# Kernel tuning notes

Measured on AMD Instinct MI355X. Metric: run time of the kernel, lower is better.

## Reference

```python
import jax, jax.numpy as jnp
import numpy as np


def setup_inputs() -> dict:
    key = jax.random.key(0)
    k1, k2, k3 = jax.random.split(key, 3)
    B, C, H, W = 8, 256, 64, 64
    K = jax.random.normal(k1, (B, C, H, W), dtype=jnp.float32)
    Q = jax.random.normal(k2, (B, C, H, W), dtype=jnp.float32)
    V = jax.random.normal(k3, (B, C, H, W), dtype=jnp.float32)
    return {"K": K, "Q": Q, "V": V}


def reference(K, Q, V):
    # K, Q: [b, dim, h, w]; V: [b, v_dim, h, w]
    b, dim, h, w = K.shape
    v_dim = V.shape[1]
    hw = h * w
    Qf = jnp.transpose(K.reshape(b, dim, hw), (0, 2, 1)) * 0  # placeholder removed below
    Qf = jnp.transpose(Q.reshape(b, dim, hw), (0, 2, 1))  # [b, hw, dim]
    Kf = K.reshape(b, dim, hw)                              # [b, dim, hw]
    Vf = jnp.transpose(V.reshape(b, v_dim, hw), (0, 2, 1))  # [b, hw, v_dim]
    scores = jnp.einsum('bqd,bdk->bqk', Qf, Kf)             # [b, hw_q, hw_k]
    # NOTE: softmax over the QUERY axis (dim=1), matching the torch code
    att = jax.nn.softmax(scores, axis=1)
    out = jnp.einsum('bqk,bkv->bqv', att, Vf)               # [b, hw, v_dim]
    out = out.reshape(b, h, w, v_dim)
    return jnp.transpose(out, (0, 3, 1, 2))                 # [b, v_dim, h, w]
```

## Files before the change

### kernel.cpp

```cpp
#include <hip/hip_runtime.h>

#define HW   4096
#define DIM  256
#define NB   8

typedef short bf16x8 __attribute__((ext_vector_type(8)));
typedef short s16x4  __attribute__((ext_vector_type(4)));
typedef float f32x4  __attribute__((ext_vector_type(4)));
typedef float f32x16 __attribute__((ext_vector_type(16)));
typedef unsigned int u32;
typedef unsigned int u32_g __attribute__((address_space(1)));
typedef unsigned int u32_l __attribute__((address_space(3)));

__device__ __forceinline__ void split_bf16(float x, short& hi, short& lo) {
    unsigned u  = __builtin_bit_cast(unsigned, x);
    unsigned rh = (u + 0x7FFFu + ((u >> 16) & 1u)) >> 16;
    hi = (short)rh;
    float hf  = __builtin_bit_cast(float, rh << 16);
    float rem = x - hf;
    unsigned u2 = __builtin_bit_cast(unsigned, rem);
    unsigned rl = (u2 + 0x7FFFu + ((u2 >> 16) & 1u)) >> 16;
    lo = (short)rl;
}

__device__ __forceinline__ f32x4 mfma16(bf16x8 a, bf16x8 b, f32x4 c) {
    return __builtin_amdgcn_mfma_f32_16x16x32_bf16(a, b, c, 0, 0, 0);
}
__device__ __forceinline__ f32x16 mfma32(bf16x8 a, bf16x8 b, f32x16 c) {
    return __builtin_amdgcn_mfma_f32_32x32x16_bf16(a, b, c, 0, 0, 0);
}

__device__ __forceinline__ void gload16(const void* g, void* l) {
    __builtin_amdgcn_global_load_lds((const u32_g*)g, (u32_l*)l, 16, 0, 0);
}


extern "C" __global__ void __launch_bounds__(256)
pass0_T(const float* __restrict__ src, short* __restrict__ dsth,
        short* __restrict__ dstl)
{
    __shared__ __attribute__((aligned(16))) short TH[16][264];
    __shared__ __attribute__((aligned(16))) short TL[16][264];
    const int b   = blockIdx.y;
    const int hw0 = blockIdx.x * 16;
    const int t   = threadIdx.x;
    const float* sb = src + (size_t)b * DIM * HW;

    {
        const int rl = t & 15;
        const int dl = t >> 4;
        #pragma unroll
        for (int dp = 0; dp < 16; ++dp) {
            int d = dl + dp * 16;
            float x = sb[(size_t)d * HW + hw0 + rl];
            short h, l; split_bf16(x, h, l);
            TH[rl][d] = h; TL[rl][d] = l;
        }
    }
    __syncthreads();

    const int r   = t >> 4;
    const int c0  = (t & 15) * 2;
    const int swz = (r & 7) << 4;
    size_t rowbyte = ((size_t)b * HW + hw0 + r) * (size_t)(DIM * 2);
    char* dh = (char*)dsth + rowbyte;
    char* dl = (char*)dstl + rowbyte;
    #pragma unroll
    for (int j = 0; j < 2; ++j) {
        int cb  = (c0 + j) * 16;
        int cbs = cb ^ swz;
        *(f32x4*)(dh + cbs) = *(const f32x4*)((const char*)&TH[r][0] + cb);
        *(f32x4*)(dl + cbs) = *(const f32x4*)((const char*)&TL[r][0] + cb);
    }
}

extern "C" __global__ void __launch_bounds__(256)
pass0_V(const float* __restrict__ V, short* __restrict__ v2)
{
    const int b = blockIdx.y, v = blockIdx.x, t = threadIdx.x;
    const float* sv = V + ((size_t)b * DIM + v) * HW + t * 16;
    #pragma unroll
    for (int s = 0; s < 2; ++s) {
        f32x4 x0 = *(const f32x4*)(sv + s * 8);
        f32x4 x1 = *(const f32x4*)(sv + s * 8 + 4);
        s16x4 h0, l0, h1, l1;
        #pragma unroll
        for (int j = 0; j < 4; ++j) {
            short h, l;
            split_bf16(x0[j], h, l); h0[j] = h; l0[j] = l;
            split_bf16(x1[j], h, l); h1[j] = h; l1[j] = l;
        }
        short* dp = v2 + (((size_t)b * 512 + (size_t)(t * 2 + s)) * DIM + v) * 16;
        *(s16x4*)(dp + 0)  = h0;
        *(s16x4*)(dp + 4)  = h1;
        *(s16x4*)(dp + 8)  = l0;
        *(s16x4*)(dp + 12) = l1;
    }
}

extern "C" __global__ void __launch_bounds__(256, 2)
k2_stats(const short* __restrict__ KTh, const short* __restrict__ KTl,
         const short* __restrict__ QTh, const short* __restrict__ QTl,
         float* __restrict__ m_out, float* __restrict__ il_out)
{
    __shared__ __attribute__((aligned(16))) short QH[2][32][256];
    __shared__ __attribute__((aligned(16))) short QL[2][32][256];

    const int b    = blockIdx.y;
    const int k0b  = blockIdx.x * 64;
    const int t    = threadIdx.x;
    const int lane = t & 63;
    const int w    = t >> 6;
    const int g    = lane >> 4;
    const int lq   = lane & 15;

    bf16x8 kh[8], kl[8];
    {
        const int krow = k0b + w * 16 + lq;
        const char* rh = (const char*)KTh + ((size_t)b * HW + krow) * 512;
        const char* rl = (const char*)KTl + ((size_t)b * HW + krow) * 512;
        const int swz = (lq & 7) << 4;
        #pragma unroll
        for (int ds = 0; ds < 8; ++ds) {
            int cb = (64 * ds + 16 * g) ^ swz;
            kh[ds] = *(const bf16x8*)(rh + cb);
            kl[ds] = *(const bf16x8*)(rl + cb);
        }
    }

    const char* qhbase = (const char*)QTh + (size_t)b * HW * 512;
    const char* qlbase = (const char*)QTl + (size_t)b * HW * 512;
    auto stage = [&](int bi, int q0) {
        #pragma unroll
        for (int j = 0; j < 4; ++j) {
            int c   = (j << 2) + w;
            int off = c * 1024 + lane * 16;
            gload16(qhbase + (size_t)q0 * 512 + off, (char*)&QH[bi][0][0] + c * 1024);
            gload16(qlbase + (size_t)q0 * 512 + off, (char*)&QL[bi][0][0] + c * 1024);
        }
    };

    float mr[4], lr[4];
    #pragma unroll
    for (int r = 0; r < 4; ++r) { mr[r] = -3.0e38f; lr[r] = 0.0f; }

    stage(0, 0);
    __syncthreads();

    for (int it = 0; it < 128; ++it) {
        const int cur = it & 1;
        if (it + 1 < 128) stage(cur ^ 1, (it + 1) * 32);

        #pragma unroll
        for (int qt = 0; qt < 2; ++qt) {
            const int qr = qt * 16 + lq;
            const char* bhr = (const char*)&QH[cur][qr][0];
            const char* blr = (const char*)&QL[cur][qr][0];
            const int swzq = (qr & 7) << 4;
            f32x4 acc = {0.f, 0.f, 0.f, 0.f};
            #pragma unroll
            for (int ds = 0; ds < 8; ++ds) {
                int cb = (64 * ds + 16 * g) ^ swzq;
                bf16x8 bh = *(const bf16x8*)(bhr + cb);
                bf16x8 bl = *(const bf16x8*)(blr + cb);
                acc = mfma16(kh[ds], bh, acc);
                acc = mfma16(kh[ds], bl, acc);
                acc = mfma16(kl[ds], bh, acc);
            }
            #pragma unroll
            for (int r = 0; r < 4; ++r) {
                float s = acc[r];
                if (s > mr[r]) {
                    lr[r] = lr[r] * __expf(mr[r] - s) + 1.0f;
                    mr[r] = s;
                } else {
                    lr[r] += __expf(s - mr[r]);
                }
            }
        }
        __syncthreads();
    }

    #pragma unroll
    for (int r = 0; r < 4; ++r) {
        float m = mr[r], l = lr[r];
        #pragma unroll
        for (int off = 1; off < 16; off <<= 1) {
            float m2 = __shfl_xor(m, off);
            float l2 = __shfl_xor(l, off);
            float mn = fmaxf(m, m2);
            l = l * __expf(m - mn) + l2 * __expf(m2 - mn);
            m = mn;
        }
        if (lq == 0) {
            int kg = k0b + w * 16 + g * 4 + r;
            m_out[b * HW + kg]  = m;
            il_out[b * HW + kg] = 1.0f / l;
        }
    }
}

extern "C" __global__ void __launch_bounds__(256, 2)
k2_out(const short* __restrict__ KTh, const short* __restrict__ KTl,
       const short* __restrict__ QTh, const short* __restrict__ QTl,
       const short* __restrict__ V2,
       const float* __restrict__ m_in, const float* __restrict__ il_in,
       float* __restrict__ out)
{
    __shared__ __attribute__((aligned(16))) short KH[2][32][256];
    __shared__ __attribute__((aligned(16))) short KL[2][32][256];
    __shared__ __attribute__((aligned(16))) short PH[64][32];
    __shared__ __attribute__((aligned(16))) short PL[64][32];

    const int b    = blockIdx.y;
    const int q0   = blockIdx.x * 64;
    const int t    = threadIdx.x;
    const int lane = t & 63;
    const int w    = t >> 6;
    const int g    = lane >> 4;
    const int lq   = lane & 15;
    const int g2   = lane >> 5;
    const int l32  = lane & 31;

    bf16x8 qh[8], ql[8];
    {
        const int qrow = q0 + w * 16 + lq;
        const char* rh = (const char*)QTh + ((size_t)b * HW + qrow) * 512;
        const char* rl = (const char*)QTl + ((size_t)b * HW + qrow) * 512;
        const int swz = (lq & 7) << 4;
        #pragma unroll
        for (int ds = 0; ds < 8; ++ds) {
            int cb = (64 * ds + 16 * g) ^ swz;
            qh[ds] = *(const bf16x8*)(rh + cb);
            ql[ds] = *(const bf16x8*)(rl + cb);
        }
    }

    const char* khbase = (const char*)KTh + (size_t)b * HW * 512;
    const char* klbase = (const char*)KTl + (size_t)b * HW * 512;
    auto stage = [&](int bi, int k0) {
        #pragma unroll
        for (int j = 0; j < 4; ++j) {
            int c   = (j << 2) + w;
            int off = c * 1024 + lane * 16;
            gload16(khbase + (size_t)k0 * 512 + off, (char*)&KH[bi][0][0] + c * 1024);
            gload16(klbase + (size_t)k0 * 512 + off, (char*)&KL[bi][0][0] + c * 1024);
        }
    };

    f32x16 acc[2][2];
    #pragma unroll
    for (int i = 0; i < 2; ++i)
        #pragma unroll
        for (int j = 0; j < 2; ++j)
            #pragma unroll
            for (int e = 0; e < 16; ++e) acc[i][j][e] = 0.0f;

    const float* mB  = m_in  + b * HW;
    const float* ilB = il_in + b * HW;

    stage(0, 0);
    __syncthreads();

    for (int it = 0; it < 128; ++it) {
        const int cur = it & 1;
        const int k0  = it * 32;
        if (it + 1 < 128) stage(cur ^ 1, k0 + 32);

        f32x4 sacc[2];
        #pragma unroll
        for (int kt = 0; kt < 2; ++kt) { f32x4 z = {0.f,0.f,0.f,0.f}; sacc[kt] = z; }
        const int swzk = (lq & 7) << 4;
        const char* ahr0 = (const char*)&KH[cur][lq][0];
        const char* ahr1 = (const char*)&KH[cur][16 + lq][0];
        const char* alr0 = (const char*)&KL[cur][lq][0];
        const char* alr1 = (const char*)&KL[cur][16 + lq][0];
        #pragma unroll
        for (int ds = 0; ds < 8; ++ds) {
            int cb = (64 * ds + 16 * g) ^ swzk;
            {
                bf16x8 ah = *(const bf16x8*)(ahr0 + cb);
                bf16x8 al = *(const bf16x8*)(alr0 + cb);
                sacc[0] = mfma16(ah, qh[ds], sacc[0]);
                sacc[0] = mfma16(ah, ql[ds], sacc[0]);
                sacc[0] = mfma16(al, qh[ds], sacc[0]);
            }
            {
                bf16x8 ah = *(const bf16x8*)(ahr1 + cb);
                bf16x8 al = *(const bf16x8*)(alr1 + cb);
                sacc[1] = mfma16(ah, qh[ds], sacc[1]);
                sacc[1] = mfma16(ah, ql[ds], sacc[1]);
                sacc[1] = mfma16(al, qh[ds], sacc[1]);
            }
        }

        {
            const int qc   = w * 16 + lq;
            const int pswz = ((qc >> 1) & 3) << 4;
            #pragma unroll
            for (int kt = 0; kt < 2; ++kt) {
                int kg = k0 + kt * 16 + g * 4;
                f32x4 m4  = *(const f32x4*)&mB[kg];
                f32x4 il4 = *(const f32x4*)&ilB[kg];
                s16x4 ph, pl;
                #pragma unroll
                for (int r = 0; r < 4; ++r) {
                    float p = __expf(sacc[kt][r] - m4[r]) * il4[r];
                    short h, l; split_bf16(p, h, l);
                    ph[r] = h; pl[r] = l;
                }
                int cb = (32 * kt + 8 * g) ^ pswz;
                *(s16x4*)((char*)&PH[0][0] + qc * 64 + cb) = ph;
                *(s16x4*)((char*)&PL[0][0] + qc * 64 + cb) = pl;
            }
        }
        __syncthreads();

        #pragma unroll
        for (int kc = 0; kc < 2; ++kc) {
            bf16x8 pbh[2], pbl[2];
            #pragma unroll
            for (int qt = 0; qt < 2; ++qt) {
                int prow = qt * 32 + l32;
                int cb = (32 * kc + 16 * g2) ^ (((prow >> 1) & 3) << 4);
                pbh[qt] = *(const bf16x8*)((const char*)&PH[0][0] + prow * 64 + cb);
                pbl[qt] = *(const bf16x8*)((const char*)&PL[0][0] + prow * 64 + cb);
            }
            const int seg = (k0 >> 3) + kc * 2 + g2;
            #pragma unroll
            for (int mt = 0; mt < 2; ++mt) {
                int v = w * 64 + mt * 32 + l32;
                const short* vp = V2 + (((size_t)b * 512 + seg) * DIM + v) * 16;
                bf16x8 vh = *(const bf16x8*)(vp);
                bf16x8 vl = *(const bf16x8*)(vp + 8);
                #pragma unroll
                for (int qt = 0; qt < 2; ++qt) {
                    acc[mt][qt] = mfma32(vh, pbh[qt], acc[mt][qt]);
                    acc[mt][qt] = mfma32(vh, pbl[qt], acc[mt][qt]);
                    acc[mt][qt] = mfma32(vl, pbh[qt], acc[mt][qt]);
                }
            }
        }
        __syncthreads();
    }

    float* ob = out + (size_t)b * DIM * HW;
    #pragma unroll
    for (int mt = 0; mt < 2; ++mt)
        #pragma unroll
        for (int qt = 0; qt < 2; ++qt)
            #pragma unroll
            for (int r = 0; r < 16; ++r) {
                int v = w * 64 + mt * 32 + (r & 3) + 8 * (r >> 2) + 4 * g2;
                int q = q0 + qt * 32 + l32;
                ob[(size_t)v * HW + q] = acc[mt][qt][r];
            }
}

extern "C" __global__ void __launch_bounds__(256, 1)
k_stats(const float* __restrict__ K, const float* __restrict__ Q,
        float* __restrict__ m_out, float* __restrict__ il_out)
{
    __shared__ __attribute__((aligned(16))) short KtH[64][264];
    __shared__ __attribute__((aligned(16))) short KtL[64][264];
    __shared__ __attribute__((aligned(16))) short QtH[32][264];
    __shared__ __attribute__((aligned(16))) short QtL[32][264];

    const int b = blockIdx.y, k0 = blockIdx.x * 64, t = threadIdx.x;
    const int lane = t & 63, w = t >> 6, g = lane >> 4, lq = lane & 15;
    const float* Kb = K + (size_t)b * DIM * HW;
    const float* Qb = Q + (size_t)b * DIM * HW;

    {
        const int kk = t & 63, d0 = t >> 6;
        #pragma unroll 4
        for (int pass = 0; pass < 64; ++pass) {
            int d = d0 + pass * 4;
            float x = Kb[(size_t)d * HW + k0 + kk];
            short h, l; split_bf16(x, h, l);
            KtH[kk][d] = h; KtL[kk][d] = l;
        }
    }
    float mr[4], lr[4];
    #pragma unroll
    for (int r = 0; r < 4; ++r) { mr[r] = -3.0e38f; lr[r] = 0.0f; }

    for (int q0 = 0; q0 < HW; q0 += 32) {
        __syncthreads();
        {
            const int qq = t & 31, d0 = t >> 5;
            #pragma unroll 4
            for (int pass = 0; pass < 32; ++pass) {
                int d = d0 + pass * 8;
                float x = Qb[(size_t)d * HW + q0 + qq];
                short h, l; split_bf16(x, h, l);
                QtH[qq][d] = h; QtL[qq][d] = l;
            }
        }
        __syncthreads();
        #pragma unroll
        for (int qt = 0; qt < 2; ++qt) {
            f32x4 acc = {0.f, 0.f, 0.f, 0.f};
            #pragma unroll
            for (int ds = 0; ds < 8; ++ds) {
                const int dof = ds * 32 + g * 8;
                bf16x8 ah = *(const bf16x8*)&KtH[w * 16 + lq][dof];
                bf16x8 al = *(const bf16x8*)&KtL[w * 16 + lq][dof];
                bf16x8 bh = *(const bf16x8*)&QtH[qt * 16 + lq][dof];
                bf16x8 bl = *(const bf16x8*)&QtL[qt * 16 + lq][dof];
                acc = mfma16(ah, bh, acc);
                acc = mfma16(ah, bl, acc);
                acc = mfma16(al, bh, acc);
            }
            #pragma unroll
            for (int r = 0; r < 4; ++r) {
                float s = acc[r];
                if (s > mr[r]) { lr[r] = lr[r] * __expf(mr[r] - s) + 1.0f; mr[r] = s; }
                else lr[r] += __expf(s - mr[r]);
            }
        }
    }
    #pragma unroll
    for (int r = 0; r < 4; ++r) {
        float m = mr[r], l = lr[r];
        #pragma unroll
        for (int off = 1; off < 16; off <<= 1) {
            float m2 = __shfl_xor(m, off), l2 = __shfl_xor(l, off);
            float mn = fmaxf(m, m2);
            l = l * __expf(m - mn) + l2 * __expf(m2 - mn);
            m = mn;
        }
        if (lq == 0) {
            int kg = k0 + w * 16 + g * 4 + r;
            m_out[b * HW + kg] = m;
            il_out[b * HW + kg] = 1.0f / l;
        }
    }
}

extern "C" __global__ void __launch_bounds__(256, 1)
k_attn_out(const float* __restrict__ K, const float* __restrict__ Q,
           const float* __restrict__ V,
           const float* __restrict__ m_in, const float* __restrict__ il_in,
           float* __restrict__ out)
{
    __shared__ __attribute__((aligned(16))) short QtH[64][264];
    __shared__ __attribute__((aligned(16))) short QtL[64][264];
    __shared__ __attribute__((aligned(16))) short KtH[32][264];
    __shared__ __attribute__((aligned(16))) short KtL[32][264];
    __shared__ __attribute__((aligned(16))) short PtH[64][40];
    __shared__ __attribute__((aligned(16))) short PtL[64][40];

    const int b = blockIdx.y, q0 = blockIdx.x * 64, t = threadIdx.x;
    const int lane = t & 63, w = t >> 6, g = lane >> 4, lq = lane & 15;
    const int g2 = lane >> 5, l32 = lane & 31;
    const float* Kb = K + (size_t)b * DIM * HW;
    const float* Qb = Q + (size_t)b * DIM * HW;
    const float* Vb = V + (size_t)b * DIM * HW;
    const float* mB = m_in + b * HW;
    const float* ilB = il_in + b * HW;

    {
        const int qq = t & 63, d0 = t >> 6;
        #pragma unroll 4
        for (int pass = 0; pass < 64; ++pass) {
            int d = d0 + pass * 4;
            float x = Qb[(size_t)d * HW + q0 + qq];
            short h, l; split_bf16(x, h, l);
            QtH[qq][d] = h; QtL[qq][d] = l;
        }
    }
    f32x16 acc[2][2];
    #pragma unroll
    for (int i = 0; i < 2; ++i)
        #pragma unroll
        for (int j = 0; j < 2; ++j)
            #pragma unroll
            for (int e = 0; e < 16; ++e) acc[i][j][e] = 0.0f;

    for (int k0 = 0; k0 < HW; k0 += 32) {
        __syncthreads();
        {
            const int kk = t & 31, d0 = t >> 5;
            #pragma unroll 4
            for (int pass = 0; pass < 32; ++pass) {
                int d = d0 + pass * 8;
                float x = Kb[(size_t)d * HW + k0 + kk];
                short h, l; split_bf16(x, h, l);
                KtH[kk][d] = h; KtL[kk][d] = l;
            }
        }
        __syncthreads();
        f32x4 sacc[2];
        #pragma unroll
        for (int kt = 0; kt < 2; ++kt) { f32x4 z = {0.f,0.f,0.f,0.f}; sacc[kt] = z; }
        #pragma unroll
        for (int ds = 0; ds < 8; ++ds) {
            const int dof = ds * 32 + g * 8;
            bf16x8 bh = *(const bf16x8*)&QtH[w * 16 + lq][dof];
            bf16x8 bl = *(const bf16x8*)&QtL[w * 16 + lq][dof];
            #pragma unroll
            for (int kt = 0; kt < 2; ++kt) {
                bf16x8 ah = *(const bf16x8*)&KtH[kt * 16 + lq][dof];
                bf16x8 al = *(const bf16x8*)&KtL[kt * 16 + lq][dof];
                sacc[kt] = mfma16(ah, bh, sacc[kt]);
                sacc[kt] = mfma16(ah, bl, sacc[kt]);
                sacc[kt] = mfma16(al, bh, sacc[kt]);
            }
        }
        {
            const int qc = w * 16 + lq;
            #pragma unroll
            for (int kt = 0; kt < 2; ++kt) {
                s16x4 ph, pl;
                #pragma unroll
                for (int r = 0; r < 4; ++r) {
                    int kg = k0 + kt * 16 + g * 4 + r;
                    float p = __expf(sacc[kt][r] - mB[kg]) * ilB[kg];
                    short h, l; split_bf16(p, h, l);
                    ph[r] = h; pl[r] = l;
                }
                *(s16x4*)&PtH[qc][kt * 16 + g * 4] = ph;
                *(s16x4*)&PtL[qc][kt * 16 + g * 4] = pl;
            }
        }
        __syncthreads();
        #pragma unroll
        for (int kc = 0; kc < 2; ++kc) {
            bf16x8 pbh[2], pbl[2];
            #pragma unroll
            for (int qt = 0; qt < 2; ++qt) {
                pbh[qt] = *(const bf16x8*)&PtH[qt * 32 + l32][kc * 16 + g2 * 8];
                pbl[qt] = *(const bf16x8*)&PtL[qt * 32 + l32][kc * 16 + g2 * 8];
            }
            #pragma unroll
            for (int mt = 0; mt < 2; ++mt) {
                const int v = w * 64 + mt * 32 + l32;
                const float* vp = Vb + (size_t)v * HW + k0 + kc * 16 + g2 * 8;
                f32x4 x0 = *(const f32x4*)vp;
                f32x4 x1 = *(const f32x4*)(vp + 4);
                bf16x8 ah, al;
                #pragma unroll
                for (int j = 0; j < 4; ++j) {
                    short h, l;
                    split_bf16(x0[j], h, l); ah[j] = h;     al[j] = l;
                    split_bf16(x1[j], h, l); ah[4 + j] = h; al[4 + j] = l;
                }
                #pragma unroll
                for (int qt = 0; qt < 2; ++qt) {
                    acc[mt][qt] = mfma32(ah, pbh[qt], acc[mt][qt]);
                    acc[mt][qt] = mfma32(ah, pbl[qt], acc[mt][qt]);
                    acc[mt][qt] = mfma32(al, pbh[qt], acc[mt][qt]);
                }
            }
        }
    }
    float* ob = out + (size_t)b * DIM * HW;
    #pragma unroll
    for (int mt = 0; mt < 2; ++mt)
        #pragma unroll
        for (int qt = 0; qt < 2; ++qt)
            #pragma unroll
            for (int r = 0; r < 16; ++r) {
                int v = w * 64 + mt * 32 + (r & 3) + 8 * (r >> 2) + 4 * g2;
                int q = q0 + qt * 32 + l32;
                ob[(size_t)v * HW + q] = acc[mt][qt][r];
            }
}

extern "C" void kernel_launch(void* const* d_in, const int* in_sizes, int n_in,
                              void* d_out, int out_size, void* d_ws, size_t ws_size,
                              hipStream_t stream)
{
    (void)in_sizes; (void)n_in; (void)out_size;
    const float* K = (const float*)d_in[0];
    const float* Q = (const float*)d_in[1];
    const float* V = (const float*)d_in[2];

    char* wsb = (char*)d_ws;
    float* m_ws  = (float*)wsb;
    float* il_ws = m_ws + (size_t)NB * HW;

    const size_t planeElems = (size_t)NB * HW * DIM;
    const size_t statsBytes = 262144;
    const size_t need = statsBytes + planeElems * 2 * 4
                                   + planeElems * 2 * 2 ;

    dim3 blk(256);
    if (ws_size >= need) {
        short* KTh = (short*)(wsb + statsBytes);
        short* KTl = KTh + planeElems;
        short* QTh = KTl + planeElems;
        short* QTl = QTh + planeElems;
        short* V2  = QTl + planeElems;

        dim3 gT(HW / 16, NB);
        pass0_T<<<gT, blk, 0, stream>>>(K, KTh, KTl);
        pass0_T<<<gT, blk, 0, stream>>>(Q, QTh, QTl);
        dim3 gV(DIM, NB);
        pass0_V<<<gV, blk, 0, stream>>>(V, V2);

        dim3 gM(64, NB);
        k2_stats<<<gM, blk, 0, stream>>>(KTh, KTl, QTh, QTl, m_ws, il_ws);
        k2_out<<<gM, blk, 0, stream>>>(KTh, KTl, QTh, QTl, V2, m_ws, il_ws,
                                       (float*)d_out);
    } else {
        dim3 gM(64, NB);
        k_stats<<<gM, blk, 0, stream>>>(K, Q, m_ws, il_ws);
        k_attn_out<<<gM, blk, 0, stream>>>(K, Q, V, m_ws, il_ws, (float*)d_out);
    }
}
```

Before: 733.7 us.

## Use 512-thread blocks with larger tiles, double-buffered P, and MFMA priority hints

Both attention kernels move to 512-thread blocks covering 128 rows per block, and the grid is flattened with the batch index interleaved. The stats kernel stages 64 query rows per iteration, halving the loop count. The output kernel double-buffers the P tile in LDS, which removes the trailing barrier, and it prefetches the V fragments and softmax stats into registers before the score MFMAs. s_setprio is raised around the MFMA sections. This aims to improve operand reuse and latency hiding, at the cost of more registers and LDS per block, which may reduce occupancy. The swizzled P layout is also replaced by padded rows read with 8-byte loads.

```diff
diff --git a/kernel.cpp b/kernel.cpp
--- a/kernel.cpp
+++ b/kernel.cpp
@@ -33,7 +33,6 @@
 __device__ __forceinline__ void gload16(const void* g, void* l) {
     __builtin_amdgcn_global_load_lds((const u32_g*)g, (u32_l*)l, 16, 0, 0);
 }
-
 
 extern "C" __global__ void __launch_bounds__(256)
 pass0_T(const float* __restrict__ src, short* __restrict__ dsth,
@@ -98,16 +97,17 @@
     }
 }
 
-extern "C" __global__ void __launch_bounds__(256, 2)
-k2_stats(const short* __restrict__ KTh, const short* __restrict__ KTl,
+extern "C" __global__ void __launch_bounds__(512, 2)
+k3_stats(const short* __restrict__ KTh, const short* __restrict__ KTl,
          const short* __restrict__ QTh, const short* __restrict__ QTl,
          float* __restrict__ m_out, float* __restrict__ il_out)
 {
-    __shared__ __attribute__((aligned(16))) short QH[2][32][256];
-    __shared__ __attribute__((aligned(16))) short QL[2][32][256];
-
-    const int b    = blockIdx.y;
-    const int k0b  = blockIdx.x * 64;
+    __shared__ __attribute__((aligned(16))) short QH[2][64][256];
+    __shared__ __attribute__((aligned(16))) short QL[2][64][256];
+
+    const int id   = blockIdx.x;
+    const int b    = id & 7;
+    const int k0b  = (id >> 3) * 128;
     const int t    = threadIdx.x;
     const int lane = t & 63;
     const int w    = t >> 6;
@@ -133,10 +133,12 @@
     auto stage = [&](int bi, int q0) {
         #pragma unroll
         for (int j = 0; j < 4; ++j) {
-            int c   = (j << 2) + w;
-            int off = c * 1024 + lane * 16;
-            gload16(qhbase + (size_t)q0 * 512 + off, (char*)&QH[bi][0][0] + c * 1024);
-            gload16(qlbase + (size_t)q0 * 512 + off, (char*)&QL[bi][0][0] + c * 1024);
+            int c = (j << 3) + w;
+            int o = c * 1024;
+            gload16(qhbase + (size_t)q0 * 512 + o + lane * 16,
+                    (char*)&QH[bi][0][0] + o);
+            gload16(qlbase + (size_t)q0 * 512 + o + lane * 16,
+                    (char*)&QL[bi][0][0] + o);
         }
     };
 
@@ -147,17 +149,18 @@
     stage(0, 0);
     __syncthreads();
 
-    for (int it = 0; it < 128; ++it) {
+    for (int it = 0; it < 64; ++it) {
         const int cur = it & 1;
-        if (it + 1 < 128) stage(cur ^ 1, (it + 1) * 32);
-
-        #pragma unroll
-        for (int qt = 0; qt < 2; ++qt) {
+        if (it + 1 < 64) stage(cur ^ 1, (it + 1) * 64);
+
+        #pragma unroll
+        for (int qt = 0; qt < 4; ++qt) {
             const int qr = qt * 16 + lq;
             const char* bhr = (const char*)&QH[cur][qr][0];
             const char* blr = (const char*)&QL[cur][qr][0];
             const int swzq = (qr & 7) << 4;
             f32x4 acc = {0.f, 0.f, 0.f, 0.f};
+            __builtin_amdgcn_s_setprio(1);
             #pragma unroll
             for (int ds = 0; ds < 8; ++ds) {
                 int cb = (64 * ds + 16 * g) ^ swzq;
@@ -167,6 +170,7 @@
                 acc = mfma16(kh[ds], bl, acc);
                 acc = mfma16(kl[ds], bh, acc);
             }
+            __builtin_amdgcn_s_setprio(0);
             #pragma unroll
             for (int r = 0; r < 4; ++r) {
                 float s = acc[r];
@@ -200,8 +204,8 @@
     }
 }
 
-extern "C" __global__ void __launch_bounds__(256, 2)
-k2_out(const short* __restrict__ KTh, const short* __restrict__ KTl,
+extern "C" __global__ void __launch_bounds__(512, 2)
+k3_out(const short* __restrict__ KTh, const short* __restrict__ KTl,
        const short* __restrict__ QTh, const short* __restrict__ QTl,
        const short* __restrict__ V2,
        const float* __restrict__ m_in, const float* __restrict__ il_in,
@@ -209,11 +213,12 @@
 {
     __shared__ __attribute__((aligned(16))) short KH[2][32][256];
     __shared__ __attribute__((aligned(16))) short KL[2][32][256];
-    __shared__ __attribute__((aligned(16))) short PH[64][32];
-    __shared__ __attribute__((aligned(16))) short PL[64][32];
-
-    const int b    = blockIdx.y;
-    const int q0   = blockIdx.x * 64;
+    __shared__ __attribute__((aligned(16))) short PH[2][128][36];
+    __shared__ __attribute__((aligned(16))) short PL[2][128][36];
+
+    const int id   = blockIdx.x;
+    const int b    = id & 7;
+    const int q0   = (id >> 3) * 128;
     const int t    = threadIdx.x;
     const int lane = t & 63;
     const int w    = t >> 6;
@@ -221,6 +226,8 @@
     const int lq   = lane & 15;
     const int g2   = lane >> 5;
     const int l32  = lane & 31;
+    const int wv   = w >> 1;
+    const int wq2  = w & 1;
 
     bf16x8 qh[8], ql[8];
     {
@@ -238,13 +245,15 @@
 
     const char* khbase = (const char*)KTh + (size_t)b * HW * 512;
     const char* klbase = (const char*)KTl + (size_t)b * HW * 512;
-    auto stage = [&](int bi, int k0) {
-        #pragma unroll
-        for (int j = 0; j < 4; ++j) {
-            int c   = (j << 2) + w;
-            int off = c * 1024 + lane * 16;
-            gload16(khbase + (size_t)k0 * 512 + off, (char*)&KH[bi][0][0] + c * 1024);
-            gload16(klbase + (size_t)k0 * 512 + off, (char*)&KL[bi][0][0] + c * 1024);
+    auto stage = [&](int bi, int k0a) {
+        #pragma unroll
+        for (int j = 0; j < 2; ++j) {
+            int c = (j << 3) + w;
+            int o = c * 1024;
+            gload16(khbase + (size_t)k0a * 512 + o + lane * 16,
+                    (char*)&KH[bi][0][0] + o);
+            gload16(klbase + (size_t)k0a * 512 + o + lane * 16,
+                    (char*)&KL[bi][0][0] + o);
         }
     };
 
@@ -265,7 +274,28 @@
     for (int it = 0; it < 128; ++it) {
         const int cur = it & 1;
         const int k0  = it * 32;
+
         if (it + 1 < 128) stage(cur ^ 1, k0 + 32);
+
+        f32x4 mv[2], iv[2];
+        #pragma unroll
+        for (int kt = 0; kt < 2; ++kt) {
+            mv[kt] = *(const f32x4*)&mB[k0 + kt * 16 + g * 4];
+            iv[kt] = *(const f32x4*)&ilB[k0 + kt * 16 + g * 4];
+        }
+
+        bf16x8 vfh[2][2], vfl[2][2];
+        #pragma unroll
+        for (int kc = 0; kc < 2; ++kc) {
+            const int seg = (k0 >> 3) + kc * 2 + g2;
+            #pragma unroll
+            for (int mt = 0; mt < 2; ++mt) {
+                const int v = wv * 64 + mt * 32 + l32;
+                const short* vp = V2 + (((size_t)b * 512 + seg) * DIM + v) * 16;
+                vfh[kc][mt] = *(const bf16x8*)(vp);
+                vfl[kc][mt] = *(const bf16x8*)(vp + 8);
+            }
+        }
 
         f32x4 sacc[2];
         #pragma unroll
@@ -275,6 +305,7 @@
         const char* ahr1 = (const char*)&KH[cur][16 + lq][0];
         const char* alr0 = (const char*)&KL[cur][lq][0];
         const char* alr1 = (const char*)&KL[cur][16 + lq][0];
+        __builtin_amdgcn_s_setprio(1);
         #pragma unroll
         for (int ds = 0; ds < 8; ++ds) {
             int cb = (64 * ds + 16 * g) ^ swzk;
@@ -293,66 +324,69 @@
                 sacc[1] = mfma16(al, qh[ds], sacc[1]);
             }
         }
+        __builtin_amdgcn_s_setprio(0);
 
         {
-            const int qc   = w * 16 + lq;
-            const int pswz = ((qc >> 1) & 3) << 4;
+            const int qc = w * 16 + lq;
             #pragma unroll
             for (int kt = 0; kt < 2; ++kt) {
-                int kg = k0 + kt * 16 + g * 4;
-                f32x4 m4  = *(const f32x4*)&mB[kg];
-                f32x4 il4 = *(const f32x4*)&ilB[kg];
                 s16x4 ph, pl;
                 #pragma unroll
                 for (int r = 0; r < 4; ++r) {
-                    float p = __expf(sacc[kt][r] - m4[r]) * il4[r];
+                    float p = __expf(sacc[kt][r] - mv[kt][r]) * iv[kt][r];
                     short h, l; split_bf16(p, h, l);
                     ph[r] = h; pl[r] = l;
                 }
-                int cb = (32 * kt + 8 * g) ^ pswz;
-                *(s16x4*)((char*)&PH[0][0] + qc * 64 + cb) = ph;
-                *(s16x4*)((char*)&PL[0][0] + qc * 64 + cb) = pl;
-            }
-        }
+                *(s16x4*)&PH[cur][qc][kt * 16 + g * 4] = ph;
+                *(s16x4*)&PL[cur][qc][kt * 16 + g * 4] = pl;
+            }
+        }
+
         __syncthreads();
 
+        __builtin_amdgcn_s_setprio(1);
         #pragma unroll
         for (int kc = 0; kc < 2; ++kc) {
             bf16x8 pbh[2], pbl[2];
             #pragma unroll
             for (int qt = 0; qt < 2; ++qt) {
-                int prow = qt * 32 + l32;
-                int cb = (32 * kc + 16 * g2) ^ (((prow >> 1) & 3) << 4);
-                pbh[qt] = *(const bf16x8*)((const char*)&PH[0][0] + prow * 64 + cb);
-                pbl[qt] = *(const bf16x8*)((const char*)&PL[0][0] + prow * 64 + cb);
-            }
-            const int seg = (k0 >> 3) + kc * 2 + g2;
+                const int prow = wq2 * 64 + qt * 32 + l32;
+                const short* p0 = &PH[cur][prow][kc * 16 + g2 * 8];
+                const short* p1 = &PL[cur][prow][kc * 16 + g2 * 8];
+                s16x4 a0 = *(const s16x4*)(p0);
+                s16x4 a1 = *(const s16x4*)(p0 + 4);
+                s16x4 b0 = *(const s16x4*)(p1);
+                s16x4 b1 = *(const s16x4*)(p1 + 4);
+                bf16x8 rh, rl;
+                #pragma unroll
+                for (int e = 0; e < 4; ++e) {
+                    rh[e] = a0[e]; rh[4 + e] = a1[e];
+                    rl[e] = b0[e]; rl[4 + e] = b1[e];
+                }
+                pbh[qt] = rh; pbl[qt] = rl;
+            }
             #pragma unroll
             for (int mt = 0; mt < 2; ++mt) {
-                int v = w * 64 + mt * 32 + l32;
-                const short* vp = V2 + (((size_t)b * 512 + seg) * DIM + v) * 16;
-                bf16x8 vh = *(const bf16x8*)(vp);
-                bf16x8 vl = *(const bf16x8*)(vp + 8);
                 #pragma unroll
                 for (int qt = 0; qt < 2; ++qt) {
-                    acc[mt][qt] = mfma32(vh, pbh[qt], acc[mt][qt]);
-                    acc[mt][qt] = mfma32(vh, pbl[qt], acc[mt][qt]);
-                    acc[mt][qt] = mfma32(vl, pbh[qt], acc[mt][qt]);
+                    acc[mt][qt] = mfma32(vfh[kc][mt], pbh[qt], acc[mt][qt]);
+                    acc[mt][qt] = mfma32(vfh[kc][mt], pbl[qt], acc[mt][qt]);
+                    acc[mt][qt] = mfma32(vfl[kc][mt], pbh[qt], acc[mt][qt]);
                 }
             }
         }
-        __syncthreads();
-    }
-
-    float* ob = out + (size_t)b * DIM * HW;
+        __builtin_amdgcn_s_setprio(0);
+    }
+
+    float* __restrict__ ob = out + (size_t)b * DIM * HW;
     #pragma unroll
     for (int mt = 0; mt < 2; ++mt)
         #pragma unroll
         for (int qt = 0; qt < 2; ++qt)
             #pragma unroll
             for (int r = 0; r < 16; ++r) {
-                int v = w * 64 + mt * 32 + (r & 3) + 8 * (r >> 2) + 4 * g2;
-                int q = q0 + qt * 32 + l32;
+                int v = wv * 64 + mt * 32 + (r & 3) + 8 * (r >> 2) + 4 * g2;
+                int q = q0 + wq2 * 64 + qt * 32 + l32;
                 ob[(size_t)v * HW + q] = acc[mt][qt][r];
             }
 }
@@ -600,10 +634,10 @@
         dim3 gV(DIM, NB);
         pass0_V<<<gV, blk, 0, stream>>>(V, V2);
 
-        dim3 gM(64, NB);
-        k2_stats<<<gM, blk, 0, stream>>>(KTh, KTl, QTh, QTl, m_ws, il_ws);
-        k2_out<<<gM, blk, 0, stream>>>(KTh, KTl, QTh, QTl, V2, m_ws, il_ws,
-                                       (float*)d_out);
+        dim3 blk5(512);
+        k3_stats<<<dim3(256), blk5, 0, stream>>>(KTh, KTl, QTh, QTl, m_ws, il_ws);
+        k3_out<<<dim3(256), blk5, 0, stream>>>(KTh, KTl, QTh, QTl, V2,
+                                               m_ws, il_ws, (float*)d_out);
     } else {
         dim3 gM(64, NB);
         k_stats<<<gM, blk, 0, stream>>>(K, Q, m_ws, il_ws);
```

Result: faster. 638.3 us (-13.0%).
